# Kernel optimization log

Measured on AMD Instinct MI355X. Metric: run time of the kernel, lower is better.

## Reference

```python
import jax, jax.numpy as jnp
import numpy as np
from jax import lax

K_SIZE = 5  # dilated_kernel_size


def dcls_kernel(w, p, k=K_SIZE):
    """Build dense (Cout,Cin,k,k) kernel from DCLS v1 bilinear interpolation.
    w: (Cout,Cin,Kc) weights; p: (2,Cout,Cin,Kc) learnable positions."""
    lim = k // 2
    pos = jnp.clip(p, -lim, lim) + lim          # in [0, k-1]
    i = jnp.floor(pos).astype(jnp.int32)
    r = pos - i                                  # bilinear fractions
    Co, Ci, Kc = w.shape
    co = jnp.arange(Co)[:, None, None]
    ci = jnp.arange(Ci)[None, :, None]
    i1, i2 = i[0], i[1]
    r1, r2 = r[0], r[1]
    # scatter into (k+1)x(k+1) grid so i+1 never goes out of bounds, then trim
    K = jnp.zeros((Co, Ci, k + 1, k + 1), w.dtype)
    K = K.at[co, ci, i1,     i2    ].add(w * (1 - r1) * (1 - r2))
    K = K.at[co, ci, i1 + 1, i2    ].add(w * r1 * (1 - r2))
    K = K.at[co, ci, i1,     i2 + 1].add(w * (1 - r1) * r2)
    K = K.at[co, ci, i1 + 1, i2 + 1].add(w * r1 * r2)
    return K[:, :, :k, :k]


def conv2d(x, K, pad):
    return lax.conv_general_dilated(
        x, K, window_strides=(1, 1), padding=[(pad, pad), (pad, pad)],
        dimension_numbers=('NCHW', 'OIHW', 'NCHW'))


def maxpool2(x):
    return lax.reduce_window(x, -jnp.inf, lax.max, (1, 1, 2, 2), (1, 1, 2, 2), 'VALID')


def setup_inputs() -> dict:
    key = jax.random.key(0)
    ks = jax.random.split(key, 12)
    lim = K_SIZE // 2
    B = 4096
    x = jax.random.normal(ks[0], (B, 1, 28, 28), jnp.float32)
    w1 = jax.random.normal(ks[1], (32, 1, 16), jnp.float32) * 0.2
    p1 = jax.random.uniform(ks[2], (2, 32, 1, 16), jnp.float32, -lim, lim)
    b1 = jnp.zeros((32,), jnp.float32)
    w2 = jax.random.normal(ks[3], (64, 32, 32), jnp.float32) * 0.05
    p2 = jax.random.uniform(ks[4], (2, 64, 32, 32), jnp.float32, -lim, lim)
    b2 = jnp.zeros((64,), jnp.float32)
    fc1_w = jax.random.normal(ks[5], (128, 64 * 7 * 7), jnp.float32) * 0.02
    fc1_b = jnp.zeros((128,), jnp.float32)
    fc2_w = jax.random.normal(ks[6], (10, 128), jnp.float32) * 0.08
    fc2_b = jnp.zeros((10,), jnp.float32)
    return dict(x=x, w1=w1, p1=p1, b1=b1, w2=w2, p2=p2, b2=b2,
                fc1_w=fc1_w, fc1_b=fc1_b, fc2_w=fc2_w, fc2_b=fc2_b)


def reference(x, w1, p1, b1, w2, p2, b2, fc1_w, fc1_b, fc2_w, fc2_b):
    h = conv2d(x, dcls_kernel(w1, p1), pad=2) + b1[None, :, None, None]
    h = maxpool2(jax.nn.relu(h))                       # (B,32,14,14)
    h = conv2d(h, dcls_kernel(w2, p2), pad=2) + b2[None, :, None, None]
    h = maxpool2(jax.nn.relu(h))                       # (B,64,7,7)
    h = h.reshape(-1, 64 * 7 * 7)
    h = jax.nn.relu(h @ fc1_w.T + fc1_b)
    return h @ fc2_w.T + fc2_b                         # (B,10)
```

## Files before the change

### kernel.cpp

```cpp
#include <hip/hip_runtime.h>
#include <hip/hip_bf16.h>

typedef __attribute__((ext_vector_type(8))) short short8;
typedef __attribute__((ext_vector_type(4))) short short4v;
typedef __attribute__((ext_vector_type(4))) float float4v;
typedef __attribute__((ext_vector_type(16))) float float16v;

static __device__ __forceinline__ unsigned short f2bf(float f) {
    unsigned u = __float_as_uint(f);
    unsigned r = (u + 0x7FFF + ((u >> 16) & 1)) >> 16;
    return (unsigned short)r;
}

__global__ __launch_bounds__(256) void prep_all(
    const float* __restrict__ w1, const float* __restrict__ p1,
    const float* __restrict__ w2, const float* __restrict__ p2,
    const float* __restrict__ fc1w,
    unsigned short* __restrict__ K1b,
    unsigned short* __restrict__ Kt,
    unsigned short* __restrict__ w1b) {
    const int blk = blockIdx.x;
    const int t = threadIdx.x;

    if (blk < 8) {
        int cell = blk * 256 + t;
        int co = cell >> 6;
        int k = cell & 63;
        int wr = k >> 3;
        int kx = k & 7;
        float acc = 0.f;
        if (wr < 5 && kx < 5) {
#pragma unroll 8
            for (int kc = 0; kc < 16; ++kc) {
                float wv = w1[co * 16 + kc];
                float pa = p1[co * 16 + kc];
                float pb = p1[512 + co * 16 + kc];
                float pos1 = fminf(fmaxf(pa, -2.f), 2.f) + 2.f;
                float pos2 = fminf(fmaxf(pb, -2.f), 2.f) + 2.f;
                int i1 = (int)floorf(pos1);
                int i2 = (int)floorf(pos2);
                float r1 = pos1 - (float)i1;
                float r2 = pos2 - (float)i2;
                float c = 0.f;
                if (i1 == wr && i2 == kx) c += (1.f - r1) * (1.f - r2);
                if (i1 + 1 == wr && i2 == kx) c += r1 * (1.f - r2);
                if (i1 == wr && i2 + 1 == kx) c += (1.f - r1) * r2;
                if (i1 + 1 == wr && i2 + 1 == kx) c += r1 * r2;
                acc += wv * c;
            }
        }
        K1b[cell] = f2bf(acc);
    } else if (blk < 208) {
        int cell = (blk - 8) * 256 + t;
        int kk = cell >> 11;
        int co = (cell >> 5) & 63;
        int ci = cell & 31;
        int ky = kk / 5;
        int kx = kk - 5 * ky;
        const int base = (co * 32 + ci) * 32;
        float acc = 0.f;
#pragma unroll 8
        for (int kc = 0; kc < 32; ++kc) {
            float wv = w2[base + kc];
            float pa = p2[base + kc];
            float pb = p2[65536 + base + kc];
            float pos1 = fminf(fmaxf(pa, -2.f), 2.f) + 2.f;
            float pos2 = fminf(fmaxf(pb, -2.f), 2.f) + 2.f;
            int i1 = (int)floorf(pos1);
            int i2 = (int)floorf(pos2);
            float r1 = pos1 - (float)i1;
            float r2 = pos2 - (float)i2;
            float c = 0.f;
            if (i1 == ky && i2 == kx) c += (1.f - r1) * (1.f - r2);
            if (i1 + 1 == ky && i2 == kx) c += r1 * (1.f - r2);
            if (i1 == ky && i2 + 1 == kx) c += (1.f - r1) * r2;
            if (i1 + 1 == ky && i2 + 1 == kx) c += r1 * r2;
            acc += wv * c;
        }
        Kt[cell] = f2bf(acc);
    } else {
        int i8 = ((blk - 208) * 256 + t) * 8;
        float4 v0 = *(const float4*)(fc1w + i8);
        float4 v1 = *(const float4*)(fc1w + i8 + 4);
        short8 o = {(short)f2bf(v0.x), (short)f2bf(v0.y), (short)f2bf(v0.z),
                    (short)f2bf(v0.w), (short)f2bf(v1.x), (short)f2bf(v1.y),
                    (short)f2bf(v1.z), (short)f2bf(v1.w)};
        *(short8*)(w1b + i8) = o;
    }
}

__global__ __launch_bounds__(256, 4) void fused_conv_mfma(
    const float* __restrict__ x,
    const unsigned short* __restrict__ K1b,
    const unsigned short* __restrict__ Kt,
    const float* __restrict__ b1,
    const float* __restrict__ b2,
    unsigned short* __restrict__ h2) {
    __shared__ __align__(16) unsigned short h1p[18 * 20 * 40];
    __shared__ __align__(16) unsigned short sm4[4 * 29 * 44];
    __shared__ __align__(16) unsigned short sm_xb[784];

    const int b = blockIdx.x;
    const int tid = threadIdx.x;
    const int lane = tid & 63;
    const int wv = tid >> 6;
    const int n16 = lane & 15;
    const int cig = lane >> 4;

    const int yi = 2 * (n16 >> 3) + ((n16 >> 1) & 1);
    const int xi = 2 * ((n16 >> 2) & 1) + (n16 & 1);
    const int pYo = cig >> 1, pXo = cig & 1;

    const int mq = lane & 31;
    const int Qx = mq >> 2;
    const int dy2 = (mq >> 1) & 1;
    const int dx2 = mq & 1;
    const int hh = lane >> 5;

    for (int t = tid; t < 1800; t += 256) ((uint4*)h1p)[t] = uint4{0, 0, 0, 0};
    {
        const float* xb = x + (size_t)b * 784;
        for (int t = tid; t < 784; t += 256) sm_xb[t] = f2bf(xb[t]);
    }
    __syncthreads();

    if (tid < 116) {
        int s = tid / 29;
        int r = tid - s * 29;
        unsigned short* dst = sm4 + (s * 29 + r) * 44;
        bool rok = r < 28;
#pragma unroll
        for (int g = 0; g < 11; ++g) {
            short4v v;
#pragma unroll
            for (int e = 0; e < 4; ++e) {
                int c = g * 4 + e + s - 4;
                v[e] = (short)((rok && (unsigned)c < 28u) ? sm_xb[r * 28 + c]
                                                          : (unsigned short)0);
            }
            *(short4v*)(dst + g * 4) = v;
        }
    }

    short8 bw[2][2];
    float bias1[2], bias2n[2];
#pragma unroll
    for (int cot = 0; cot < 2; ++cot) {
#pragma unroll
        for (int h = 0; h < 2; ++h)
            bw[cot][h] = *(const short8*)(K1b + (cot * 16 + n16) * 64 + h * 32 + cig * 8);
        bias1[cot] = b1[cot * 16 + n16];
    }
#pragma unroll
    for (int nt = 0; nt < 2; ++nt) bias2n[nt] = b2[nt * 32 + mq];

    const int s1 = (xi + 2) & 3;
    const int pb1 = (xi + 2) & ~3;
    const unsigned short* a1base = sm4 + s1 * (29 * 44) + pb1;

    __syncthreads();

    for (int i = 0; i < 13; ++i) {
        int t = wv + 4 * i;
        if (t < 49) {
            int tY = t / 7, tX = t - 7 * tY;
            const unsigned short* ab = a1base + 4 * tX;
            int r0 = 4 * tY + yi - 2 + cig;
            int r1 = r0 + 4;
            int rr0 = ((unsigned)r0 < 28u) ? r0 : 28;
            int rr1 = ((unsigned)r1 < 28u) ? r1 : 28;
            short4v lo0 = *(const short4v*)(ab + rr0 * 44);
            short4v hi0 = *(const short4v*)(ab + rr0 * 44 + 4);
            short4v lo1 = *(const short4v*)(ab + rr1 * 44);
            short4v hi1 = *(const short4v*)(ab + rr1 * 44 + 4);
            short8 af0 = {lo0[0], lo0[1], lo0[2], lo0[3], hi0[0], hi0[1], hi0[2], hi0[3]};
            short8 af1 = {lo1[0], lo1[1], lo1[2], lo1[3], hi1[0], hi1[1], hi1[2], hi1[3]};
            int pY = 2 * tY + pYo, pX = 2 * tX + pXo;
#pragma unroll
            for (int cot = 0; cot < 2; ++cot) {
                float4v acc = {0.f, 0.f, 0.f, 0.f};
                acc = __builtin_amdgcn_mfma_f32_16x16x32_bf16(af0, bw[cot][0], acc, 0, 0, 0);
                acc = __builtin_amdgcn_mfma_f32_16x16x32_bf16(af1, bw[cot][1], acc, 0, 0, 0);
                float v = fmaxf(fmaxf(acc[0], acc[1]), fmaxf(acc[2], acc[3]));
                v = fmaxf(v + bias1[cot], 0.f);
                h1p[((pY + 2) * 20 + (pX + 2)) * 40 + cot * 16 + n16] = f2bf(v);
            }
        }
    }
    __syncthreads();

    int x2 = 2 * Qx + dx2;
    if (x2 > 13) x2 = 13;
    int aoff[2][2];
    int pYv[2];
#pragma unroll
    for (int mt = 0; mt < 2; ++mt) {
        int pY = 2 * wv + mt;
        int y2 = 2 * pY + dy2;
        if (y2 > 13) y2 = 13;
        pYv[mt] = pY;
#pragma unroll
        for (int kh2 = 0; kh2 < 2; ++kh2)
            aoff[mt][kh2] = (y2 * 20 + x2) * 40 + kh2 * 16 + hh * 8;
    }

    float16v acc2[2][2];
#pragma unroll
    for (int mt = 0; mt < 2; ++mt)
#pragma unroll
        for (int nt = 0; nt < 2; ++nt)
#pragma unroll
            for (int e = 0; e < 16; ++e) acc2[mt][nt][e] = 0.f;

#pragma unroll
    for (int ky = 0; ky < 5; ++ky) {
#pragma unroll
        for (int kx = 0; kx < 5; ++kx) {
            int kk = ky * 5 + kx;
            short8 wf[2][2];
#pragma unroll
            for (int nt = 0; nt < 2; ++nt)
#pragma unroll
                for (int kh2 = 0; kh2 < 2; ++kh2)
                    wf[nt][kh2] = *(const short8*)(Kt + kk * 2048 +
                        (nt * 32 + mq) * 32 + kh2 * 16 + hh * 8);
#pragma unroll
            for (int mt = 0; mt < 2; ++mt) {
                short8 af0 = *(const short8*)(h1p + aoff[mt][0] + (ky * 20 + kx) * 40);
                short8 af1 = *(const short8*)(h1p + aoff[mt][1] + (ky * 20 + kx) * 40);
#pragma unroll
                for (int nt = 0; nt < 2; ++nt) {
                    acc2[mt][nt] = __builtin_amdgcn_mfma_f32_32x32x16_bf16(
                        af0, wf[nt][0], acc2[mt][nt], 0, 0, 0);
                    acc2[mt][nt] = __builtin_amdgcn_mfma_f32_32x32x16_bf16(
                        af1, wf[nt][1], acc2[mt][nt], 0, 0, 0);
                }
            }
        }
    }

    unsigned short* outb = h2 + (size_t)b * 3136;
#pragma unroll
    for (int mt = 0; mt < 2; ++mt) {
        if (pYv[mt] < 7) {
#pragma unroll
            for (int nt = 0; nt < 2; ++nt) {
#pragma unroll
                for (int g = 0; g < 4; ++g) {
                    int pX = 2 * g + hh;
                    float v = fmaxf(fmaxf(acc2[mt][nt][4 * g], acc2[mt][nt][4 * g + 1]),
                                    fmaxf(acc2[mt][nt][4 * g + 2], acc2[mt][nt][4 * g + 3]));
                    v = fmaxf(v + bias2n[nt], 0.f);
                    if (pX < 7)
                        outb[(nt * 32 + mq) * 49 + pYv[mt] * 7 + pX] = f2bf(v);
                }
            }
        }
    }
}

__global__ __launch_bounds__(256) void fc1_mfma(
    const unsigned short* __restrict__ A,
    const unsigned short* __restrict__ Wb,
    float* __restrict__ part, size_t PB) {
    __shared__ __align__(16) unsigned short As[64 * 72];
    const int blk = blockIdx.x;
    const int kh = blk % 7;
    const int m0 = (blk / 7) * 64;
    const int tid = threadIdx.x;
    const int wv = tid >> 6;
    const int lane = tid & 63;
    const int n16 = lane & 15;
    const int cig = lane >> 4;

    float4v acc[4][2];
#pragma unroll
    for (int mt = 0; mt < 4; ++mt)
#pragma unroll
        for (int j = 0; j < 2; ++j) acc[mt][j] = float4v{0.f, 0.f, 0.f, 0.f};

    for (int it = 0; it < 7; ++it) {
        int k0 = kh * 448 + it * 64;
        __syncthreads();
#pragma unroll
        for (int i = 0; i < 2; ++i) {
            int p = tid + 256 * i;
            int r = p >> 3, ko = (p & 7) * 8;
            *(short8*)(As + r * 72 + ko) =
                *(const short8*)(A + (size_t)(m0 + r) * 3136 + k0 + ko);
        }
        __syncthreads();
#pragma unroll
        for (int h = 0; h < 2; ++h) {
            short8 af[4];
#pragma unroll
            for (int mt = 0; mt < 4; ++mt)
                af[mt] = *(const short8*)(As + (mt * 16 + n16) * 72 + h * 32 + cig * 8);
            short8 wf[2];
#pragma unroll
            for (int j = 0; j < 2; ++j)
                wf[j] = *(const short8*)(Wb + (size_t)((wv * 2 + j) * 16 + n16) * 3136 +
                                         k0 + h * 32 + cig * 8);
#pragma unroll
            for (int mt = 0; mt < 4; ++mt)
#pragma unroll
                for (int j = 0; j < 2; ++j)
                    acc[mt][j] = __builtin_amdgcn_mfma_f32_16x16x32_bf16(
                        af[mt], wf[j], acc[mt][j], 0, 0, 0);
        }
    }
    float* o = part + (size_t)kh * PB;
#pragma unroll
    for (int mt = 0; mt < 4; ++mt)
#pragma unroll
        for (int j = 0; j < 2; ++j)
#pragma unroll
            for (int r = 0; r < 4; ++r) {
                int row = m0 + mt * 16 + cig * 4 + r;
                o[(size_t)row * 128 + (wv * 2 + j) * 16 + n16] = acc[mt][j][r];
            }
}

__global__ __launch_bounds__(256) void fc2_kernel(
    const float* __restrict__ part, size_t PB,
    const float* __restrict__ fc1b,
    const float* __restrict__ W, const float* __restrict__ bias,
    float* __restrict__ out) {
    __shared__ float smW[10 * 132];
    __shared__ float smB1[128];
    __shared__ float smB[10];
    int t = threadIdx.x;
    for (int i = t; i < 1280; i += 256) {
        int n = i >> 7, k = i & 127;
        smW[n * 132 + k] = W[i];
    }
    if (t < 128) smB1[t] = fc1b[t];
    if (t < 10) smB[t] = bias[t];
    __syncthreads();
    const int r = t >> 3;
    const int q = t & 7;
    const size_t b = (size_t)blockIdx.x * 32 + r;
    const float* pb = part + b * 128 + q * 16;

    float rv[16];
#pragma unroll
    for (int c = 0; c < 4; ++c) {
        float4 s = *(const float4*)(pb + 4 * c);
#pragma unroll
        for (int j = 1; j < 7; ++j) {
            float4 pj = *(const float4*)(pb + (size_t)j * PB + 4 * c);
            s.x += pj.x; s.y += pj.y; s.z += pj.z; s.w += pj.w;
        }
        float4 bv = *(const float4*)(smB1 + q * 16 + 4 * c);
        rv[4 * c + 0] = fmaxf(s.x + bv.x, 0.f);
        rv[4 * c + 1] = fmaxf(s.y + bv.y, 0.f);
        rv[4 * c + 2] = fmaxf(s.z + bv.z, 0.f);
        rv[4 * c + 3] = fmaxf(s.w + bv.w, 0.f);
    }
    float acc[10];
#pragma unroll
    for (int n = 0; n < 10; ++n) {
        const float4* wr = (const float4*)(smW + n * 132 + q * 16);
        float a = 0.f;
#pragma unroll
        for (int c = 0; c < 4; ++c) {
            float4 w = wr[c];
            a += rv[4 * c] * w.x + rv[4 * c + 1] * w.y +
                 rv[4 * c + 2] * w.z + rv[4 * c + 3] * w.w;
        }
        acc[n] = a;
    }
#pragma unroll
    for (int n = 0; n < 10; ++n) {
        acc[n] += __shfl_xor(acc[n], 1);
        acc[n] += __shfl_xor(acc[n], 2);
        acc[n] += __shfl_xor(acc[n], 4);
    }
    if (q == 0) {
#pragma unroll
        for (int n = 0; n < 10; ++n) out[b * 10 + n] = acc[n] + smB[n];
    }
}

extern "C" void kernel_launch(void* const* d_in, const int* in_sizes, int n_in,
                              void* d_out, int out_size, void* d_ws, size_t ws_size,
                              hipStream_t stream) {
    const float* x    = (const float*)d_in[0];
    const float* w1   = (const float*)d_in[1];
    const float* p1   = (const float*)d_in[2];
    const float* b1   = (const float*)d_in[3];
    const float* w2   = (const float*)d_in[4];
    const float* p2   = (const float*)d_in[5];
    const float* b2   = (const float*)d_in[6];
    const float* fc1w = (const float*)d_in[7];
    const float* fc1b = (const float*)d_in[8];
    const float* fc2w = (const float*)d_in[9];
    const float* fc2b = (const float*)d_in[10];
    float* out = (float*)d_out;

    const int B = in_sizes[0] / 784;

    float* ws = (float*)d_ws;
    unsigned short* Kt  = (unsigned short*)ws;
    unsigned short* K1b = (unsigned short*)(ws + 25600);
    unsigned short* w1b = (unsigned short*)(ws + 26624);
    unsigned short* h2b = (unsigned short*)(ws + 227328);
    float* fc1p = ws + 227328 + (size_t)B * 1568;

    prep_all<<<404, 256, 0, stream>>>(w1, p1, w2, p2, fc1w, K1b, Kt, w1b);
    fused_conv_mfma<<<B, 256, 0, stream>>>(x, K1b, Kt, b1, b2, h2b);
    fc1_mfma<<<(B / 64) * 7, 256, 0, stream>>>(h2b, w1b, fc1p, (size_t)B * 128);
    fc2_kernel<<<B / 32, 256, 0, stream>>>(fc1p, (size_t)B * 128,
                                           fc1b, fc2w, fc2b, out);
}
```

Before: 224.9 us.

## Use 512-thread blocks and remap conv2 tiles to dense pooled positions

Raises the fused conv kernel to 512 threads (8 waves) and reassigns conv2 work so each of 7 waves handles 8 consecutive pooled output positions with a single M-tile. Before, it used 2 M-tiles per wave over 8 padded rows, which wasted work on out-of-range positions. It also shrinks the padded LDS buffers (row stride 20→18, sm4 stride 44→36) and parallelizes the sm4 shifted-copy build across all threads. The aim is less wasted MFMA work and LDS use, and more occupancy. In exchange, one wave sits idle during conv2 and per-block register and LDS pressure changes under the new launch bounds.

```diff
diff --git a/kernel.cpp b/kernel.cpp
--- a/kernel.cpp
+++ b/kernel.cpp
@@ -89,15 +89,15 @@
     }
 }
 
-__global__ __launch_bounds__(256, 4) void fused_conv_mfma(
+__global__ __launch_bounds__(512, 6) void fused_conv_mfma(
     const float* __restrict__ x,
     const unsigned short* __restrict__ K1b,
     const unsigned short* __restrict__ Kt,
     const float* __restrict__ b1,
     const float* __restrict__ b2,
     unsigned short* __restrict__ h2) {
-    __shared__ __align__(16) unsigned short h1p[18 * 20 * 40];
-    __shared__ __align__(16) unsigned short sm4[4 * 29 * 44];
+    __shared__ __align__(16) unsigned short h1p[18 * 18 * 40];
+    __shared__ __align__(16) unsigned short sm4[4 * 29 * 36];
     __shared__ __align__(16) unsigned short sm_xb[784];
 
     const int b = blockIdx.x;
@@ -112,34 +112,32 @@
     const int pYo = cig >> 1, pXo = cig & 1;
 
     const int mq = lane & 31;
-    const int Qx = mq >> 2;
+    const int qit = mq >> 2;
     const int dy2 = (mq >> 1) & 1;
     const int dx2 = mq & 1;
     const int hh = lane >> 5;
 
-    for (int t = tid; t < 1800; t += 256) ((uint4*)h1p)[t] = uint4{0, 0, 0, 0};
+    for (int t = tid; t < 1620; t += 512) ((uint4*)h1p)[t] = uint4{0, 0, 0, 0};
     {
         const float* xb = x + (size_t)b * 784;
-        for (int t = tid; t < 784; t += 256) sm_xb[t] = f2bf(xb[t]);
+        for (int t = tid; t < 784; t += 512) sm_xb[t] = f2bf(xb[t]);
     }
     __syncthreads();
 
-    if (tid < 116) {
-        int s = tid / 29;
-        int r = tid - s * 29;
-        unsigned short* dst = sm4 + (s * 29 + r) * 44;
+    for (int u = tid; u < 1044; u += 512) {
+        int s = u / 261;
+        int rem = u - s * 261;
+        int r = rem / 9;
+        int g = rem - r * 9;
         bool rok = r < 28;
-#pragma unroll
-        for (int g = 0; g < 11; ++g) {
-            short4v v;
-#pragma unroll
-            for (int e = 0; e < 4; ++e) {
-                int c = g * 4 + e + s - 4;
-                v[e] = (short)((rok && (unsigned)c < 28u) ? sm_xb[r * 28 + c]
-                                                          : (unsigned short)0);
-            }
-            *(short4v*)(dst + g * 4) = v;
-        }
+        short4v v;
+#pragma unroll
+        for (int e = 0; e < 4; ++e) {
+            int c = g * 4 + e + s - 4;
+            v[e] = (short)((rok && (unsigned)c < 28u) ? sm_xb[r * 28 + c]
+                                                      : (unsigned short)0);
+        }
+        *(short4v*)(sm4 + (s * 29 + r) * 36 + g * 4) = v;
     }
 
     short8 bw[2][2];
@@ -156,12 +154,12 @@
 
     const int s1 = (xi + 2) & 3;
     const int pb1 = (xi + 2) & ~3;
-    const unsigned short* a1base = sm4 + s1 * (29 * 44) + pb1;
+    const unsigned short* a1base = sm4 + s1 * (29 * 36) + pb1;
 
     __syncthreads();
 
-    for (int i = 0; i < 13; ++i) {
-        int t = wv + 4 * i;
+    for (int i = 0; i < 7; ++i) {
+        int t = wv + 8 * i;
         if (t < 49) {
             int tY = t / 7, tX = t - 7 * tY;
             const unsigned short* ab = a1base + 4 * tX;
@@ -169,10 +167,10 @@
             int r1 = r0 + 4;
             int rr0 = ((unsigned)r0 < 28u) ? r0 : 28;
             int rr1 = ((unsigned)r1 < 28u) ? r1 : 28;
-            short4v lo0 = *(const short4v*)(ab + rr0 * 44);
-            short4v hi0 = *(const short4v*)(ab + rr0 * 44 + 4);
-            short4v lo1 = *(const short4v*)(ab + rr1 * 44);
-            short4v hi1 = *(const short4v*)(ab + rr1 * 44 + 4);
+            short4v lo0 = *(const short4v*)(ab + rr0 * 36);
+            short4v hi0 = *(const short4v*)(ab + rr0 * 36 + 4);
+            short4v lo1 = *(const short4v*)(ab + rr1 * 36);
+            short4v hi1 = *(const short4v*)(ab + rr1 * 36 + 4);
             short8 af0 = {lo0[0], lo0[1], lo0[2], lo0[3], hi0[0], hi0[1], hi0[2], hi0[3]};
             short8 af1 = {lo1[0], lo1[1], lo1[2], lo1[3], hi1[0], hi1[1], hi1[2], hi1[3]};
             int pY = 2 * tY + pYo, pX = 2 * tX + pXo;
@@ -183,76 +181,62 @@
                 acc = __builtin_amdgcn_mfma_f32_16x16x32_bf16(af1, bw[cot][1], acc, 0, 0, 0);
                 float v = fmaxf(fmaxf(acc[0], acc[1]), fmaxf(acc[2], acc[3]));
                 v = fmaxf(v + bias1[cot], 0.f);
-                h1p[((pY + 2) * 20 + (pX + 2)) * 40 + cot * 16 + n16] = f2bf(v);
+                h1p[((pY + 2) * 18 + (pX + 2)) * 40 + cot * 16 + n16] = f2bf(v);
             }
         }
     }
     __syncthreads();
 
-    int x2 = 2 * Qx + dx2;
-    if (x2 > 13) x2 = 13;
-    int aoff[2][2];
-    int pYv[2];
-#pragma unroll
-    for (int mt = 0; mt < 2; ++mt) {
-        int pY = 2 * wv + mt;
+    if (wv < 7) {
+        int q = wv * 8 + qit;
+        int qc = (q > 48) ? 48 : q;
+        int pY = qc / 7;
+        int pX = qc - 7 * pY;
         int y2 = 2 * pY + dy2;
-        if (y2 > 13) y2 = 13;
-        pYv[mt] = pY;
-#pragma unroll
-        for (int kh2 = 0; kh2 < 2; ++kh2)
-            aoff[mt][kh2] = (y2 * 20 + x2) * 40 + kh2 * 16 + hh * 8;
-    }
-
-    float16v acc2[2][2];
-#pragma unroll
-    for (int mt = 0; mt < 2; ++mt)
+        int x2 = 2 * pX + dx2;
+        const unsigned short* Ab = h1p + (y2 * 18 + x2) * 40 + hh * 8;
+
+        float16v acc2[2];
 #pragma unroll
         for (int nt = 0; nt < 2; ++nt)
 #pragma unroll
-            for (int e = 0; e < 16; ++e) acc2[mt][nt][e] = 0.f;
-
-#pragma unroll
-    for (int ky = 0; ky < 5; ++ky) {
-#pragma unroll
-        for (int kx = 0; kx < 5; ++kx) {
-            int kk = ky * 5 + kx;
-            short8 wf[2][2];
-#pragma unroll
-            for (int nt = 0; nt < 2; ++nt)
-#pragma unroll
-                for (int kh2 = 0; kh2 < 2; ++kh2)
-                    wf[nt][kh2] = *(const short8*)(Kt + kk * 2048 +
-                        (nt * 32 + mq) * 32 + kh2 * 16 + hh * 8);
-#pragma unroll
-            for (int mt = 0; mt < 2; ++mt) {
-                short8 af0 = *(const short8*)(h1p + aoff[mt][0] + (ky * 20 + kx) * 40);
-                short8 af1 = *(const short8*)(h1p + aoff[mt][1] + (ky * 20 + kx) * 40);
+            for (int e = 0; e < 16; ++e) acc2[nt][e] = 0.f;
+
+#pragma unroll
+        for (int ky = 0; ky < 5; ++ky) {
+#pragma unroll
+            for (int kx = 0; kx < 5; ++kx) {
+                int kk = ky * 5 + kx;
+                short8 wf[2][2];
+#pragma unroll
+                for (int nt = 0; nt < 2; ++nt)
+#pragma unroll
+                    for (int kh2 = 0; kh2 < 2; ++kh2)
+                        wf[nt][kh2] = *(const short8*)(Kt + kk * 2048 +
+                            (nt * 32 + mq) * 32 + kh2 * 16 + hh * 8);
+                short8 af0 = *(const short8*)(Ab + (ky * 18 + kx) * 40);
+                short8 af1 = *(const short8*)(Ab + (ky * 18 + kx) * 40 + 16);
 #pragma unroll
                 for (int nt = 0; nt < 2; ++nt) {
-                    acc2[mt][nt] = __builtin_amdgcn_mfma_f32_32x32x16_bf16(
-                        af0, wf[nt][0], acc2[mt][nt], 0, 0, 0);
-                    acc2[mt][nt] = __builtin_amdgcn_mfma_f32_32x32x16_bf16(
-                        af1, wf[nt][1], acc2[mt][nt], 0, 0, 0);
+                    acc2[nt] = __builtin_amdgcn_mfma_f32_32x32x16_bf16(
+                        af0, wf[nt][0], acc2[nt], 0, 0, 0);
+                    acc2[nt] = __builtin_amdgcn_mfma_f32_32x32x16_bf16(
+                        af1, wf[nt][1], acc2[nt], 0, 0, 0);
                 }
             }
         }
-    }
-
-    unsigned short* outb = h2 + (size_t)b * 3136;
-#pragma unroll
-    for (int mt = 0; mt < 2; ++mt) {
-        if (pYv[mt] < 7) {
-#pragma unroll
-            for (int nt = 0; nt < 2; ++nt) {
-#pragma unroll
-                for (int g = 0; g < 4; ++g) {
-                    int pX = 2 * g + hh;
-                    float v = fmaxf(fmaxf(acc2[mt][nt][4 * g], acc2[mt][nt][4 * g + 1]),
-                                    fmaxf(acc2[mt][nt][4 * g + 2], acc2[mt][nt][4 * g + 3]));
+
+        unsigned short* outb = h2 + (size_t)b * 3136;
+#pragma unroll
+        for (int g = 0; g < 4; ++g) {
+            int q_out = wv * 8 + 2 * g + hh;
+            if (q_out < 49) {
+#pragma unroll
+                for (int nt = 0; nt < 2; ++nt) {
+                    float v = fmaxf(fmaxf(acc2[nt][4 * g], acc2[nt][4 * g + 1]),
+                                    fmaxf(acc2[nt][4 * g + 2], acc2[nt][4 * g + 3]));
                     v = fmaxf(v + bias2n[nt], 0.f);
-                    if (pX < 7)
-                        outb[(nt * 32 + mq) * 49 + pYv[mt] * 7 + pX] = f2bf(v);
+                    outb[(nt * 32 + mq) * 49 + q_out] = f2bf(v);
                 }
             }
         }
@@ -408,7 +392,7 @@
     float* fc1p = ws + 227328 + (size_t)B * 1568;
 
     prep_all<<<404, 256, 0, stream>>>(w1, p1, w2, p2, fc1w, K1b, Kt, w1b);
-    fused_conv_mfma<<<B, 256, 0, stream>>>(x, K1b, Kt, b1, b2, h2b);
+    fused_conv_mfma<<<B, 512, 0, stream>>>(x, K1b, Kt, b1, b2, h2b);
     fc1_mfma<<<(B / 64) * 7, 256, 0, stream>>>(h2b, w1b, fc1p, (size_t)B * 128);
     fc2_kernel<<<B / 32, 256, 0, stream>>>(fc1p, (size_t)B * 128,
                                            fc1b, fc2w, fc2b, out);
```

Result: slower. 307.7 us (+36.8%).
